# Performance work log

Hardware: AMD Instinct MI355X
Metric: run time of the kernel (lower is better)

The kernel has to match this reference:

```python
import jax, jax.numpy as jnp
import numpy as np

L, B, D, Di, N, H, P, K, M, V = 4, 8, 2048, 4096, 128, 64, 64, 4, 8, 50288
Cch = Di + 2 * N           # conv channels = 4352
Dout = 2 * Di + 2 * N + H  # in_proj out = 8512
EPS = 1e-5


def _rms(x, w):
    return x * jax.lax.rsqrt(jnp.mean(x * x, axis=-1, keepdims=True) + EPS) * w


def setup_inputs() -> dict:
    key = jax.random.key(0)
    ks = jax.random.split(key, 16)
    s = 0.02
    return {
        "input_ids": jax.random.randint(ks[0], (B, 1), 0, V),
        "emb": jax.random.normal(ks[1], (V, D)) * s,
        "in_proj_w": jax.random.normal(ks[2], (L, D, Dout)) * s,
        "conv_w": jax.random.normal(ks[3], (L, Cch, K)) * s,
        "conv_b": jax.random.normal(ks[4], (L, Cch)) * s,
        "A_log": jax.random.normal(ks[5], (L, H)) * 0.5,
        "dt_bias": jax.random.normal(ks[6], (L, H)) * 0.5,
        "D_param": jax.random.normal(ks[7], (L, H)) * 0.5,
        "mixer_norm_w": jnp.ones((L, Di)),
        "out_proj_w": jax.random.normal(ks[8], (L, Di, D)) * s,
        "layer_norm_w": jnp.ones((L, D)),
        "norm_f_w": jnp.ones((D,)),
        "W_mc": jax.random.normal(ks[9], (L, M + 1)).at[:, -1].set(5.0),
        "conv_state": jax.random.normal(ks[10], (L, B, Cch, K)) * 0.1,
        "ssm_state": jax.random.normal(ks[11], (L, B, H, P, N)) * 0.1,
        "cached_states": jax.random.normal(ks[12], (L, B, M, H, P, N)) * 0.1,
    }


def reference(input_ids, emb, in_proj_w, conv_w, conv_b, A_log, dt_bias, D_param,
              mixer_norm_w, out_proj_w, layer_norm_w, norm_f_w, W_mc,
              conv_state, ssm_state, cached_states):
    ids = input_ids[:, 0]              # (B,)
    res = emb[ids]                     # (B, D) token embedding gather
    for l in range(L):
        xn = _rms(res, layer_norm_w[l])
        zxbcdt = xn @ in_proj_w[l]     # (B, Dout)
        z = zxbcdt[:, :Di]
        xBC = zxbcdt[:, Di:Di + Cch]
        dt = zxbcdt[:, Di + Cch:]
        # circular conv-state shift + depthwise conv over kernel dim
        cs = jnp.concatenate([conv_state[l][:, :, 1:], xBC[:, :, None]], axis=-1)
        xBC = jax.nn.silu(jnp.sum(cs * conv_w[l][None], axis=-1) + conv_b[l])
        x, Bm, Cm = xBC[:, :Di], xBC[:, Di:Di + N], xBC[:, Di + N:]
        dt = jax.nn.softplus(dt + dt_bias[l])                 # (B, H)
        dA = jnp.exp(dt * (-jnp.exp(A_log[l])))               # (B, H)
        x = x.reshape(B, H, P)
        dBx = jnp.einsum('bh,bn,bhp->bhpn', dt, Bm, x)        # (B,H,P,N)
        ssm = ssm_state[l] * dA[:, :, None, None] + dBx       # (B,H,P,N)
        # softmax-weighted fusion of cached segment states + current state
        w = jax.nn.softmax(W_mc[l])                           # (M+1,)
        fused = jnp.einsum('bmhpn,m->bhpn', cached_states[l], w[:-1]) + w[-1] * ssm
        y = jnp.einsum('bhpn,bn->bhp', fused, Cm) + D_param[l][None, :, None] * x
        y = y.reshape(B, Di)
        y = _rms(y * jax.nn.silu(z), mixer_norm_w[l])         # gated RMSNorm
        res = res + y @ out_proj_w[l]
    res = _rms(res, norm_f_w)
    logits = res @ emb.T               # tied lm_head
    return logits[:, None, :]          # (B, 1, V)
```

## Files before the change

kernel.cpp:

```cpp
#include <hip/hip_runtime.h>
#include <hip/hip_bf16.h>
#include <math.h>

#define LN 4
#define B_ 8
#define D_ 2048
#define DI 4096
#define N_ 128
#define H_ 64
#define P_ 64
#define K_ 4
#define M_ 8
#define V_ 50288
#define CCH (DI + 2*N_)
#define DOUT (2*DI + 2*N_ + H_)
#define EPSF 1e-5f
#define KT_IN 32
#define KT_OUT 128

typedef float f32x4 __attribute__((ext_vector_type(4)));

__device__ inline float wave_sum(float v) {
  #pragma unroll
  for (int off = 32; off > 0; off >>= 1) v += __shfl_xor(v, off, 64);
  return v;
}

__device__ inline float fold_reduce8(const float a[8], int lane) {
  float t0[4];
  #pragma unroll
  for (int r = 0; r < 4; ++r) {
    float keep = (lane & 1) ? a[2*r+1] : a[2*r];
    float send = (lane & 1) ? a[2*r]   : a[2*r+1];
    t0[r] = keep + __shfl_xor(send, 1, 64);
  }
  float t1[2];
  #pragma unroll
  for (int r = 0; r < 2; ++r) {
    float keep = (lane & 2) ? t0[2*r+1] : t0[2*r];
    float send = (lane & 2) ? t0[2*r]   : t0[2*r+1];
    t1[r] = keep + __shfl_xor(send, 2, 64);
  }
  float keep = (lane & 4) ? t1[1] : t1[0];
  float send = (lane & 4) ? t1[0] : t1[1];
  float u = keep + __shfl_xor(send, 4, 64);
  u += __shfl_xor(u, 8, 64);
  u += __shfl_xor(u, 16, 64);
  u += __shfl_xor(u, 32, 64);
  return u;
}

__global__ __launch_bounds__(256)
void k_prenorm(const int* __restrict__ ids, const float* __restrict__ emb,
               float* __restrict__ res, float* __restrict__ ssq_in) {
  __shared__ float lds[4];
  int b = blockIdx.x, tid = threadIdx.x;
  const float* row = emb + (size_t)ids[b] * D_;
  f32x4 v0 = *reinterpret_cast<const f32x4*>(row + tid * 8);
  f32x4 v1 = *reinterpret_cast<const f32x4*>(row + tid * 8 + 4);
  *reinterpret_cast<f32x4*>(res + (size_t)b * D_ + tid * 8)     = v0;
  *reinterpret_cast<f32x4*>(res + (size_t)b * D_ + tid * 8 + 4) = v1;
  float ss = v0[0]*v0[0] + v0[1]*v0[1] + v0[2]*v0[2] + v0[3]*v0[3]
           + v1[0]*v1[0] + v1[1]*v1[1] + v1[2]*v1[2] + v1[3]*v1[3];
  float wsum = wave_sum(ss);
  int lane = tid & 63, wid = tid >> 6;
  if (lane == 0) lds[wid] = wsum;
  __syncthreads();
  if (tid == 0) ssq_in[b] = lds[0] + lds[1] + lds[2] + lds[3];
}

__global__ __launch_bounds__(256)
void k_inproj1(const float* __restrict__ res, const float* __restrict__ ssq_in,
               const float* __restrict__ lnw, const float* __restrict__ W,
               float* __restrict__ pin) {
  __shared__ float xs[8][64];
  int tid = threadIdx.x;
  int jt = blockIdx.x % 9, kt = blockIdx.x / 9;
  int k0 = kt * 64;
  for (int i = tid; i < 8 * 64; i += 256) {
    int r = i >> 6, kk = i & 63;
    float scale = rsqrtf(ssq_in[r] / (float)D_ + EPSF);
    xs[r][kk] = res[r * D_ + k0 + kk] * scale * lnw[k0 + kk];
  }
  __syncthreads();
  int j = jt * 1024 + tid * 4;
  if (j >= DOUT) return;
  f32x4 acc[8];
  #pragma unroll
  for (int r = 0; r < 8; ++r) acc[r] = (f32x4)0.f;
  const float* Wp = W + (size_t)k0 * DOUT + j;
  for (int kk = 0; kk < 64; ++kk) {
    f32x4 w4 = __builtin_nontemporal_load(
        reinterpret_cast<const f32x4*>(Wp + (size_t)kk * DOUT));
    #pragma unroll
    for (int r = 0; r < 8; ++r) acc[r] += w4 * xs[r][kk];
  }
  #pragma unroll
  for (int r = 0; r < 8; ++r)
    *reinterpret_cast<f32x4*>(&pin[((size_t)kt * 8 + r) * DOUT + j]) = acc[r];
}

__global__ __launch_bounds__(256)
void k_inproj2_conv(const float* __restrict__ pin, const float* __restrict__ conv_state,
                    const float* __restrict__ conv_w, const float* __restrict__ conv_b,
                    const float* __restrict__ A_log, const float* __restrict__ dt_bias,
                    const float* __restrict__ W_mc,
                    float* __restrict__ zx, float* __restrict__ xbc,
                    float* __restrict__ dts, float* __restrict__ dav,
                    float* __restrict__ wmc) {
  const int TOT4 = B_ * DOUT / 4;
  int t = blockIdx.x * 256 + threadIdx.x;
  if (t >= TOT4) return;
  f32x4 s = (f32x4)0.f;
  const f32x4* p4 = reinterpret_cast<const f32x4*>(pin) + t;
  #pragma unroll 8
  for (int kt = 0; kt < KT_IN; ++kt) s += p4[(size_t)kt * TOT4];
  reinterpret_cast<f32x4*>(zx)[t] = s;
  int c4 = t * 4;
  int b = c4 / DOUT;
  int c = c4 - b * DOUT;
  #pragma unroll
  for (int e = 0; e < 4; ++e) {
    int ce = c + e;
    if (ce >= DI && ce < DI + CCH) {
      int cc = ce - DI;
      f32x4 cs4 = *reinterpret_cast<const f32x4*>(conv_state + ((size_t)b * CCH + cc) * K_);
      f32x4 cw4 = *reinterpret_cast<const f32x4*>(conv_w + (size_t)cc * K_);
      float v = cs4[1] * cw4[0] + cs4[2] * cw4[1] + cs4[3] * cw4[2]
              + s[e] * cw4[3] + conv_b[cc];
      xbc[b * CCH + cc] = v / (1.f + expf(-v));
    } else if (ce >= DI + CCH) {
      int h = ce - DI - CCH;
      float x = s[e] + dt_bias[h];
      float sp = (x > 20.f) ? x : log1pf(expf(x));
      dts[b * 64 + h] = sp;
      dav[b * 64 + h] = expf(-expf(A_log[h]) * sp);
    }
  }
  if (t == 0) {
    float mx = -1e30f;
    for (int i = 0; i < M_ + 1; ++i) mx = fmaxf(mx, W_mc[i]);
    float e2[M_ + 1], sum = 0.f;
    for (int i = 0; i < M_ + 1; ++i) { e2[i] = expf(W_mc[i] - mx); sum += e2[i]; }
    for (int i = 0; i < M_ + 1; ++i) wmc[i] = e2[i] / sum;
  }
}

__global__ __launch_bounds__(256)
void k_state(const float* __restrict__ xbc, const float* __restrict__ dts,
             const float* __restrict__ dav, const float* __restrict__ Dp_,
             const float* __restrict__ wmc, const float* __restrict__ ssm,
             const float* __restrict__ cached, float* __restrict__ y) {
  int wg = blockIdx.x * 4 + (threadIdx.x >> 6);
  int lane = threadIdx.x & 63;
  int b = wg >> 11;
  int h = (wg >> 5) & 63;
  int pp = wg & 31;
  int hf = lane >> 5, il = lane & 31;
  int p = pp * 2 + hf;
  float xv  = xbc[b * CCH + h * 64 + p];
  float dtv = dts[b * 64 + h];
  float da  = dav[b * 64 + h];
  float w8  = wmc[8];
  const f32x4* xb4 = reinterpret_cast<const f32x4*>(xbc);
  f32x4 B4 = xb4[b * (CCH / 4) + DI / 4 + il];
  f32x4 C4 = xb4[b * (CCH / 4) + DI / 4 + N_ / 4 + il];
  const f32x4* sp4 = reinterpret_cast<const f32x4*>(ssm) +
                     ((size_t)((b * H_ + h) * P_ + p)) * (N_ / 4) + il;
  const f32x4* cp4 = reinterpret_cast<const f32x4*>(cached) +
                     ((size_t)(((b * M_) * H_ + h) * P_ + p)) * (N_ / 4) + il;
  f32x4 s4 = __builtin_nontemporal_load(sp4);
  f32x4 f4 = (s4 * da + B4 * (dtv * xv)) * w8;
  #pragma unroll
  for (int m = 0; m < 8; ++m) {
    f32x4 c4 = __builtin_nontemporal_load(cp4 + (size_t)m * (H_ * P_ * N_ / 4));
    f4 += c4 * wmc[m];
  }
  f4 *= C4;
  float acc = f4[0] + f4[1] + f4[2] + f4[3];
  #pragma unroll
  for (int off = 1; off < 32; off <<= 1) acc += __shfl_xor(acc, off, 64);
  if (il == 0) y[b * DI + h * 64 + p] = acc + Dp_[h] * xv;
}

__global__ void k_gatednorm(const float* __restrict__ y, const float* __restrict__ zx,
                            const float* __restrict__ mnw, float* __restrict__ yg,
                            float* __restrict__ ssq_in) {
  __shared__ float lds[8];
  int b = blockIdx.x;
  if (threadIdx.x == 0) ssq_in[b] = 0.f;
  float tv[16];
  float ss = 0.f;
  #pragma unroll
  for (int t = 0; t < 16; ++t) {
    int i = threadIdx.x + t * 256;
    float z = zx[b * DOUT + i];
    float v = y[b * DI + i] * (z / (1.f + expf(-z)));
    tv[t] = v; ss += v * v;
  }
  float wsum = wave_sum(ss);
  int lane = threadIdx.x & 63, wid = threadIdx.x >> 6;
  if (lane == 0) lds[wid] = wsum;
  __syncthreads();
  float tot = lds[0] + lds[1] + lds[2] + lds[3];
  float scale = rsqrtf(tot / (float)DI + EPSF);
  #pragma unroll
  for (int t = 0; t < 16; ++t) {
    int i = threadIdx.x + t * 256;
    yg[b * DI + i] = tv[t] * scale * mnw[i];
  }
}

__global__ void k_outproj1(const float* __restrict__ yg, const float* __restrict__ W,
                           float* __restrict__ pout) {
  __shared__ float xs[8][32];
  int jt = blockIdx.x & 1, kt = blockIdx.x >> 1;
  int k0 = kt * 32;
  for (int i = threadIdx.x; i < 8 * 32; i += 256) {
    int r = i >> 5, kk = i & 31;
    xs[r][kk] = yg[r * DI + k0 + kk];
  }
  __syncthreads();
  int j = jt * 1024 + threadIdx.x * 4;
  f32x4 acc[8];
  #pragma unroll
  for (int r = 0; r < 8; ++r) acc[r] = (f32x4)0.f;
  const float* Wp = W + (size_t)k0 * D_ + j;
  for (int kk = 0; kk < 32; ++kk) {
    f32x4 w4 = __builtin_nontemporal_load(
        reinterpret_cast<const f32x4*>(Wp + (size_t)kk * D_));
    #pragma unroll
    for (int r = 0; r < 8; ++r) acc[r] += w4 * xs[r][kk];
  }
  #pragma unroll
  for (int r = 0; r < 8; ++r)
    *reinterpret_cast<f32x4*>(&pout[((size_t)kt * 8 + r) * D_ + j]) = acc[r];
}

__global__ __launch_bounds__(256)
void k_outproj2(const float* __restrict__ pout, float* __restrict__ res,
                float* __restrict__ ssq_in) {
  __shared__ f32x4 red[256];
  const int TOT4 = B_ * D_ / 4;
  int tid = threadIdx.x;
  int pos = blockIdx.x * 64 + (tid & 63);
  int kq = tid >> 6;
  const f32x4* p4 = reinterpret_cast<const f32x4*>(pout) + pos;
  f32x4 s = (f32x4)0.f;
  #pragma unroll 8
  for (int k = 0; k < 32; ++k)
    s += p4[(size_t)(kq * 32 + k) * TOT4];
  red[tid] = s;
  __syncthreads();
  if (tid < 64) {
    f32x4 tot = red[tid] + red[tid + 64] + red[tid + 128] + red[tid + 192];
    f32x4* r4 = reinterpret_cast<f32x4*>(res);
    f32x4 nv = r4[pos] + tot;
    r4[pos] = nv;
    float ps = nv[0]*nv[0] + nv[1]*nv[1] + nv[2]*nv[2] + nv[3]*nv[3];
    ps = wave_sum(ps);
    if (tid == 0) atomicAdd(&ssq_in[pos >> 9], ps);
  }
}

#define SL_ 4
#define KS_ (D_ / SL_)
#define NVB16 (V_ / 16)
__global__ __launch_bounds__(256)
void k_logits(const float* __restrict__ res, const float* __restrict__ ssq_in,
              const float* __restrict__ nfw, const float* __restrict__ emb,
              float* __restrict__ pl) {
  __shared__ f32x4 xs[8][KS_ / 4];
  int s = blockIdx.x & 3, vb = blockIdx.x >> 2;
  const f32x4* res4 = reinterpret_cast<const f32x4*>(res);
  const f32x4* nfw4 = reinterpret_cast<const f32x4*>(nfw);
  for (int i = threadIdx.x; i < 8 * (KS_ / 4); i += 256) {
    int r = i >> 7, q = i & 127;
    float scale = rsqrtf(ssq_in[r] / (float)D_ + EPSF);
    xs[r][q] = res4[r * (D_ / 4) + s * (KS_ / 4) + q] * scale
             * nfw4[s * (KS_ / 4) + q];
  }
  __syncthreads();
  int wid = threadIdx.x >> 6, lane = threadIdx.x & 63;
  int v0 = vb * 16 + wid * 4;
  const f32x4* e4 = reinterpret_cast<const f32x4*>(emb);
  #pragma unroll
  for (int vv = 0; vv < 4; ++vv) {
    int v = v0 + vv;
    const f32x4* ep = e4 + (size_t)v * (D_ / 4) + s * (KS_ / 4);
    float acc[8] = {0,0,0,0,0,0,0,0};
    #pragma unroll
    for (int st = 0; st < KS_ / 256; ++st) {
      int c = st * 64 + lane;
      f32x4 e = __builtin_nontemporal_load(ep + c);
      #pragma unroll
      for (int r = 0; r < 8; ++r) {
        f32x4 x = xs[r][c];
        acc[r] += e[0]*x[0] + e[1]*x[1] + e[2]*x[2] + e[3]*x[3];
      }
    }
    float u = fold_reduce8(acc, lane);
    if (lane < 8) pl[((size_t)s * 8 + lane) * V_ + v] = u;
  }
}

__global__ __launch_bounds__(256)
void k_logits2(const float* __restrict__ pl, float* __restrict__ out) {
  int v = blockIdx.x * 256 + threadIdx.x;
  if (v >= V_) return;
  int r = blockIdx.y;
  float t = pl[(size_t)r * V_ + v]
          + pl[((size_t)8  + r) * V_ + v]
          + pl[((size_t)16 + r) * V_ + v]
          + pl[((size_t)24 + r) * V_ + v];
  out[(size_t)r * V_ + v] = t;
}

extern "C" void kernel_launch(void* const* d_in, const int* in_sizes, int n_in,
                              void* d_out, int out_size, void* d_ws, size_t ws_size,
                              hipStream_t stream) {
  const int*   ids    = (const int*)  d_in[0];
  const float* emb    = (const float*)d_in[1];
  const float* inW    = (const float*)d_in[2];
  const float* convW  = (const float*)d_in[3];
  const float* convB  = (const float*)d_in[4];
  const float* Alog   = (const float*)d_in[5];
  const float* dtB    = (const float*)d_in[6];
  const float* Dpar   = (const float*)d_in[7];
  const float* mnw    = (const float*)d_in[8];
  const float* outW   = (const float*)d_in[9];
  const float* lnw    = (const float*)d_in[10];
  const float* nfw    = (const float*)d_in[11];
  const float* Wmc    = (const float*)d_in[12];
  const float* convS  = (const float*)d_in[13];
  const float* ssmS   = (const float*)d_in[14];
  const float* cached = (const float*)d_in[15];
  float* out = (float*)d_out;
  float* ws  = (float*)d_ws;

  float* res   = ws;
  float* zx    = ws + 16384;
  float* xbc   = ws + 84480;
  float* dts   = ws + 119296;
  float* dav   = ws + 119808;
  float* wmc   = ws + 120320;
  float* ssqi  = ws + 120384;
  float* y     = ws + 120448;
  float* yg    = ws + 153216;
  float* pin   = ws + 185984;
  float* pout  = ws + 2365056;
  float* pl    = ws + 4462208;

  k_prenorm<<<8, 256, 0, stream>>>(ids, emb, res, ssqi);
  for (int l = 0; l < LN; ++l) {
    k_inproj1<<<288, 256, 0, stream>>>(res, ssqi, lnw + (size_t)l * D_,
                                       inW + (size_t)l * D_ * DOUT, pin);
    k_inproj2_conv<<<67, 256, 0, stream>>>(pin,
        convS + (size_t)l * B_ * CCH * K_, convW + (size_t)l * CCH * K_,
        convB + (size_t)l * CCH, Alog + l * H_, dtB + l * H_, Wmc + l * (M_ + 1),
        zx, xbc, dts, dav, wmc);
    k_state<<<4096, 256, 0, stream>>>(xbc, dts, dav, Dpar + l * H_, wmc,
        ssmS + (size_t)l * B_ * H_ * P_ * N_,
        cached + (size_t)l * B_ * M_ * H_ * P_ * N_, y);
    k_gatednorm<<<8, 256, 0, stream>>>(y, zx, mnw + (size_t)l * DI, yg, ssqi);
    k_outproj1<<<256, 256, 0, stream>>>(yg, outW + (size_t)l * DI * D_, pout);
    k_outproj2<<<64, 256, 0, stream>>>(pout, res, ssqi);
  }
  k_logits<<<NVB16 * SL_, 256, 0, stream>>>(res, ssqi, nfw, emb, pl);
  k_logits2<<<dim3((V_ + 255) / 256, 8), 256, 0, stream>>>(pl, out);
}
```

Before: 427.9 us.

## Fuse gated RMSNorm into out-proj and rebalance in-proj column tiling

Removes the separate 8-block gated-norm kernel by having every out-proj block redundantly compute the per-row sum of squares of y*silu(z), then normalize its own 32-wide slice in shared memory. This drops one launch and the yg round trip, at the cost of each of 256 blocks re-reading all of y and z for the 8 rows and recomputing exp. The in-proj kernel now splits the 2128 float4 columns into 8 tiles of 266, so the grid drops from 288 to 256 blocks with no idle threads. In exchange, 10 threads per block handle a second column with a divergent branch.

```diff
diff --git a/kernel.cpp b/kernel.cpp
--- a/kernel.cpp
+++ b/kernel.cpp
@@ -17,6 +17,8 @@
 #define EPSF 1e-5f
 #define KT_IN 32
 #define KT_OUT 128
+#define NJ4 (DOUT / 4)
+#define JTW 266
 
 typedef float f32x4 __attribute__((ext_vector_type(4)));
 
@@ -75,7 +77,7 @@
                float* __restrict__ pin) {
   __shared__ float xs[8][64];
   int tid = threadIdx.x;
-  int jt = blockIdx.x % 9, kt = blockIdx.x / 9;
+  int jt = blockIdx.x & 7, kt = blockIdx.x >> 3;
   int k0 = kt * 64;
   for (int i = tid; i < 8 * 64; i += 256) {
     int r = i >> 6, kk = i & 63;
@@ -83,21 +85,31 @@
     xs[r][kk] = res[r * D_ + k0 + kk] * scale * lnw[k0 + kk];
   }
   __syncthreads();
-  int j = jt * 1024 + tid * 4;
-  if (j >= DOUT) return;
-  f32x4 acc[8];
-  #pragma unroll
-  for (int r = 0; r < 8; ++r) acc[r] = (f32x4)0.f;
-  const float* Wp = W + (size_t)k0 * DOUT + j;
+  int j4  = jt * JTW + tid;
+  bool two = (tid < JTW - 256);
+  int j4b = j4 + 256;
+  f32x4 acc[8], accb[8];
+  #pragma unroll
+  for (int r = 0; r < 8; ++r) { acc[r] = (f32x4)0.f; accb[r] = (f32x4)0.f; }
+  const f32x4* W4 = reinterpret_cast<const f32x4*>(W) + (size_t)k0 * NJ4;
   for (int kk = 0; kk < 64; ++kk) {
-    f32x4 w4 = __builtin_nontemporal_load(
-        reinterpret_cast<const f32x4*>(Wp + (size_t)kk * DOUT));
+    f32x4 w4 = __builtin_nontemporal_load(&W4[(size_t)kk * NJ4 + j4]);
     #pragma unroll
     for (int r = 0; r < 8; ++r) acc[r] += w4 * xs[r][kk];
+    if (two) {
+      f32x4 w4b = __builtin_nontemporal_load(&W4[(size_t)kk * NJ4 + j4b]);
+      #pragma unroll
+      for (int r = 0; r < 8; ++r) accb[r] += w4b * xs[r][kk];
+    }
   }
   #pragma unroll
   for (int r = 0; r < 8; ++r)
-    *reinterpret_cast<f32x4*>(&pin[((size_t)kt * 8 + r) * DOUT + j]) = acc[r];
+    reinterpret_cast<f32x4*>(pin)[((size_t)kt * 8 + r) * NJ4 + j4] = acc[r];
+  if (two) {
+    #pragma unroll
+    for (int r = 0; r < 8; ++r)
+      reinterpret_cast<f32x4*>(pin)[((size_t)kt * 8 + r) * NJ4 + j4b] = accb[r];
+  }
 }
 
 __global__ __launch_bounds__(256)
@@ -183,45 +195,47 @@
   if (il == 0) y[b * DI + h * 64 + p] = acc + Dp_[h] * xv;
 }
 
-__global__ void k_gatednorm(const float* __restrict__ y, const float* __restrict__ zx,
-                            const float* __restrict__ mnw, float* __restrict__ yg,
-                            float* __restrict__ ssq_in) {
-  __shared__ float lds[8];
-  int b = blockIdx.x;
-  if (threadIdx.x == 0) ssq_in[b] = 0.f;
-  float tv[16];
-  float ss = 0.f;
-  #pragma unroll
-  for (int t = 0; t < 16; ++t) {
-    int i = threadIdx.x + t * 256;
-    float z = zx[b * DOUT + i];
-    float v = y[b * DI + i] * (z / (1.f + expf(-z)));
-    tv[t] = v; ss += v * v;
-  }
-  float wsum = wave_sum(ss);
-  int lane = threadIdx.x & 63, wid = threadIdx.x >> 6;
-  if (lane == 0) lds[wid] = wsum;
-  __syncthreads();
-  float tot = lds[0] + lds[1] + lds[2] + lds[3];
-  float scale = rsqrtf(tot / (float)DI + EPSF);
-  #pragma unroll
-  for (int t = 0; t < 16; ++t) {
-    int i = threadIdx.x + t * 256;
-    yg[b * DI + i] = tv[t] * scale * mnw[i];
-  }
-}
-
-__global__ void k_outproj1(const float* __restrict__ yg, const float* __restrict__ W,
-                           float* __restrict__ pout) {
+__global__ __launch_bounds__(256)
+void k_outproj1(const float* __restrict__ y, const float* __restrict__ zx,
+                const float* __restrict__ mnw, const float* __restrict__ W,
+                float* __restrict__ pout, float* __restrict__ ssq_in) {
   __shared__ float xs[8][32];
+  __shared__ float sred[4][8];
+  int tid = threadIdx.x, lane = tid & 63, wid = tid >> 6;
+  if (blockIdx.x == 0 && tid < 8) ssq_in[tid] = 0.f;
+  const f32x4* y4 = reinterpret_cast<const f32x4*>(y);
+  const f32x4* z4 = reinterpret_cast<const f32x4*>(zx);
+  #pragma unroll
+  for (int r = 0; r < 8; ++r) {
+    float s = 0.f;
+    #pragma unroll
+    for (int t = 0; t < 4; ++t) {
+      int q = tid + t * 256;
+      f32x4 yv = y4[r * (DI / 4) + q];
+      f32x4 zv = z4[r * (DOUT / 4) + q];
+      #pragma unroll
+      for (int e = 0; e < 4; ++e) {
+        float g = zv[e] / (1.f + expf(-zv[e]));
+        float v = yv[e] * g;
+        s += v * v;
+      }
+    }
+    float wsum = wave_sum(s);
+    if (lane == 0) sred[wid][r] = wsum;
+  }
+  __syncthreads();
   int jt = blockIdx.x & 1, kt = blockIdx.x >> 1;
   int k0 = kt * 32;
-  for (int i = threadIdx.x; i < 8 * 32; i += 256) {
-    int r = i >> 5, kk = i & 31;
-    xs[r][kk] = yg[r * DI + k0 + kk];
-  }
-  __syncthreads();
-  int j = jt * 1024 + threadIdx.x * 4;
+  {
+    int r = tid >> 5, kk = tid & 31;
+    float tot = sred[0][r] + sred[1][r] + sred[2][r] + sred[3][r];
+    float scale = rsqrtf(tot / (float)DI + EPSF);
+    float z = zx[r * DOUT + k0 + kk];
+    float g = z / (1.f + expf(-z));
+    xs[r][kk] = y[r * DI + k0 + kk] * g * scale * mnw[k0 + kk];
+  }
+  __syncthreads();
+  int j = jt * 1024 + tid * 4;
   f32x4 acc[8];
   #pragma unroll
   for (int r = 0; r < 8; ++r) acc[r] = (f32x4)0.f;
@@ -346,14 +360,13 @@
   float* wmc   = ws + 120320;
   float* ssqi  = ws + 120384;
   float* y     = ws + 120448;
-  float* yg    = ws + 153216;
-  float* pin   = ws + 185984;
-  float* pout  = ws + 2365056;
-  float* pl    = ws + 4462208;
+  float* pin   = ws + 153216;
+  float* pout  = ws + 2332288;
+  float* pl    = ws + 4429440;
 
   k_prenorm<<<8, 256, 0, stream>>>(ids, emb, res, ssqi);
   for (int l = 0; l < LN; ++l) {
-    k_inproj1<<<288, 256, 0, stream>>>(res, ssqi, lnw + (size_t)l * D_,
+    k_inproj1<<<256, 256, 0, stream>>>(res, ssqi, lnw + (size_t)l * D_,
                                        inW + (size_t)l * D_ * DOUT, pin);
     k_inproj2_conv<<<67, 256, 0, stream>>>(pin,
         convS + (size_t)l * B_ * CCH * K_, convW + (size_t)l * CCH * K_,
@@ -362,8 +375,8 @@
     k_state<<<4096, 256, 0, stream>>>(xbc, dts, dav, Dpar + l * H_, wmc,
         ssmS + (size_t)l * B_ * H_ * P_ * N_,
         cached + (size_t)l * B_ * M_ * H_ * P_ * N_, y);
-    k_gatednorm<<<8, 256, 0, stream>>>(y, zx, mnw + (size_t)l * DI, yg, ssqi);
-    k_outproj1<<<256, 256, 0, stream>>>(yg, outW + (size_t)l * DI * D_, pout);
+    k_outproj1<<<256, 256, 0, stream>>>(y, zx, mnw + (size_t)l * DI,
+                                        outW + (size_t)l * DI * D_, pout, ssqi);
     k_outproj2<<<64, 256, 0, stream>>>(pout, res, ssqi);
   }
   k_logits<<<NVB16 * SL_, 256, 0, stream>>>(res, ssqi, nfw, emb, pl);
```

Result: slower. 521.6 us (+21.9%).
